# Kernel optimization log

Measured on AMD Instinct MI355X. Metric: run time of the kernel, lower is better.

The kernel has to match this reference:

```python
import jax, jax.numpy as jnp
import numpy as np

NP, NC, E, EL = 50000, 5000, 200000, 100000
DP, DC, HID, OUT, HEADS = 1280, 256, 128, 128, 4


def setup_inputs() -> dict:
    key = jax.random.key(0)
    ks = jax.random.split(key, 40)
    p = lambda k, shp: jax.random.normal(k, shp, dtype=jnp.float32) * 0.05
    inp = {
        "x_protein": jax.random.normal(ks[0], (NP, DP), dtype=jnp.float32),
        "x_class": jax.random.normal(ks[1], (NC, DC), dtype=jnp.float32),
        "src": jax.random.randint(ks[2], (E,), 0, NP),
        "dst": jax.random.randint(ks[3], (E,), 0, NC),
        "edge_label_src": jax.random.randint(ks[4], (EL,), 0, NP),
        "edge_label_dst": jax.random.randint(ks[5], (EL,), 0, NC),
        # SAGEConv, relation protein->class (updates class nodes)
        "sage_pc_Wl": p(ks[6], (DP, HID)), "sage_pc_bl": p(ks[7], (HID,)), "sage_pc_Wr": p(ks[8], (DC, HID)),
        # SAGEConv, relation class->protein (updates protein nodes)
        "sage_cp_Wl": p(ks[9], (DC, HID)), "sage_cp_bl": p(ks[10], (HID,)), "sage_cp_Wr": p(ks[11], (DP, HID)),
        # GATConv p->c (inputs are hidden after conv1)
        "gat_pc_Wsrc": p(ks[12], (HID, HEADS * HID)), "gat_pc_Wdst": p(ks[13], (HID, HEADS * HID)),
        "gat_pc_asrc": p(ks[14], (HEADS, HID)), "gat_pc_adst": p(ks[15], (HEADS, HID)), "gat_pc_b": p(ks[16], (HID,)),
        # GATConv c->p
        "gat_cp_Wsrc": p(ks[17], (HID, HEADS * HID)), "gat_cp_Wdst": p(ks[18], (HID, HEADS * HID)),
        "gat_cp_asrc": p(ks[19], (HEADS, HID)), "gat_cp_adst": p(ks[20], (HEADS, HID)), "gat_cp_b": p(ks[21], (HID,)),
        # final per-node-type Linear (to_hetero duplicates lin per node type)
        "lin_p_W": p(ks[22], (HID, OUT)), "lin_p_b": p(ks[23], (OUT,)),
        "lin_c_W": p(ks[24], (HID, OUT)), "lin_c_b": p(ks[25], (OUT,)),
        # link predictor
        "link_W": p(ks[26], (2 * OUT, 1)), "link_b": p(ks[27], (1,)),
    }
    return inp


def _sage(x_src, x_dst, s, d, Wl, bl, Wr, n_dst):
    # PyG SAGEConv: lin_l(mean_aggr(x_src)) + lin_r(x_dst); lin_l has bias.
    agg = jax.ops.segment_sum(x_src[s], d, num_segments=n_dst)
    cnt = jax.ops.segment_sum(jnp.ones((s.shape[0], 1), x_src.dtype), d, num_segments=n_dst)
    mean = agg / jnp.maximum(cnt, 1.0)
    return mean @ Wl + bl + x_dst @ Wr


def _gat(x_src, x_dst, s, d, Ws, Wd, a_s, a_d, b, n_dst):
    # PyG GATConv bipartite, heads=HEADS, concat=False, add_self_loops=False.
    H, C = a_s.shape
    hs = (x_src @ Ws).reshape(-1, H, C)   # [Ns, H, C]
    hd = (x_dst @ Wd).reshape(-1, H, C)   # [Nd, H, C]
    als = jnp.einsum('nhc,hc->nh', hs, a_s)
    ald = jnp.einsum('nhc,hc->nh', hd, a_d)
    e = jax.nn.leaky_relu(als[s] + ald[d], 0.2)                    # [E, H]
    emax = jax.ops.segment_max(e, d, num_segments=n_dst)          # stable softmax per dst
    ee = jnp.exp(e - emax[d])
    denom = jax.ops.segment_sum(ee, d, num_segments=n_dst)
    alpha = ee / denom[d]                                          # [E, H]
    out = jax.ops.segment_sum(alpha[:, :, None] * hs[s], d, num_segments=n_dst)  # [Nd, H, C]
    return out.mean(axis=1) + b  # concat=False -> mean over heads


def reference(x_protein, x_class, src, dst, edge_label_src, edge_label_dst,
              sage_pc_Wl, sage_pc_bl, sage_pc_Wr,
              sage_cp_Wl, sage_cp_bl, sage_cp_Wr,
              gat_pc_Wsrc, gat_pc_Wdst, gat_pc_asrc, gat_pc_adst, gat_pc_b,
              gat_cp_Wsrc, gat_cp_Wdst, gat_cp_asrc, gat_cp_adst, gat_cp_b,
              lin_p_W, lin_p_b, lin_c_W, lin_c_b, link_W, link_b):
    # Layer 1: hetero SAGE (each node type has exactly one incoming relation)
    h_c = jax.nn.relu(_sage(x_protein, x_class, src, dst, sage_pc_Wl, sage_pc_bl, sage_pc_Wr, NC))
    h_p = jax.nn.relu(_sage(x_class, x_protein, dst, src, sage_cp_Wl, sage_cp_bl, sage_cp_Wr, NP))
    # Layer 2: hetero GAT
    g_c = jax.nn.relu(_gat(h_p, h_c, src, dst, gat_pc_Wsrc, gat_pc_Wdst, gat_pc_asrc, gat_pc_adst, gat_pc_b, NC))
    g_p = jax.nn.relu(_gat(h_c, h_p, dst, src, gat_cp_Wsrc, gat_cp_Wdst, gat_cp_asrc, gat_cp_adst, gat_cp_b, NP))
    # Per-type output projection
    z_p = g_p @ lin_p_W + lin_p_b
    z_c = g_c @ lin_c_W + lin_c_b
    # Link predictor: gather, concat, linear, sigmoid
    ef = jnp.concatenate([z_p[edge_label_src], z_c[edge_label_dst]], axis=-1)  # [EL, 2*OUT]
    return jax.nn.sigmoid(ef @ link_W + link_b).squeeze(-1)
```

## Files before the change

### kernel.cpp

```cpp
#include <hip/hip_runtime.h>
#include <math.h>

#define NPROT 50000
#define NCLS  5000
#define DIMP  1280
#define DIMC  256
#define SCAN_N (NCLS + NPROT)

#define P1B  ((NPROT+63)/64)
#define C1BY ((NCLS+63)/64)
#define C1B  (4*C1BY)

typedef float4 f4;
typedef __attribute__((ext_vector_type(8))) short short8;
typedef __attribute__((ext_vector_type(4))) float f32x4;

__device__ __forceinline__ unsigned short f2bf(float f){
    unsigned u = __float_as_uint(f);
    u += 0x7FFFu + ((u >> 16) & 1u);
    return (unsigned short)(u >> 16);
}
__device__ __forceinline__ float bf2f(unsigned short b){
    return __uint_as_float(((unsigned)b) << 16);
}
__device__ __forceinline__ void gload_lds16(const void* g, void* l){
    __builtin_amdgcn_global_load_lds((const __attribute__((address_space(1))) void*)g,
                                     (__attribute__((address_space(3))) void*)l, 16, 0, 0);
}
__device__ __forceinline__ int OFFV(const int* __restrict__ offv, const int* __restrict__ part, int v){
    return offv[v] + part[v>>10];
}

__global__ __launch_bounds__(256) void mega1(const float* __restrict__ Af,
                                             const unsigned short* __restrict__ BtP,
                                             unsigned short* __restrict__ P1,
                                             const float* __restrict__ Ac,
                                             const float* __restrict__ WcatC,
                                             float* __restrict__ C1,
                                             const int* __restrict__ src, const int* __restrict__ dst,
                                             const int* __restrict__ offv, const int* __restrict__ part,
                                             int* __restrict__ cur, int* __restrict__ adj, int E){
    __shared__ __align__(16) unsigned char smem[24*1024];
    const int blk = blockIdx.x;
    const int tid = threadIdx.x;

    if(blk < P1B){
        unsigned char* As = smem;
        unsigned char* Bs = smem + 8*1024;
        const int lane = tid & 63;
        const int w    = tid >> 6;
        const int row0 = blk * 64;
        const int kg = lane >> 4, fr = lane & 15;

        f32x4 acc[4][4] = {};

        for(int k0 = 0; k0 < DIMP; k0 += 32){
            #pragma unroll
            for(int i=0;i<2;i++){
                int c  = i*256 + tid;
                int r  = c >> 3, cc = c & 7;
                int scc = cc ^ (r & 7);
                int srow = min(row0 + r, NPROT-1);
                gload_lds16((const void*)(Af + (size_t)srow*DIMP + k0 + scc*4),
                            (void*)(As + (i*256 + (tid & ~63))*16));
            }
            #pragma unroll
            for(int i=0;i<4;i++){
                int c  = i*256 + tid;
                int r  = c >> 2, cc = c & 3;
                int scc = cc ^ ((r>>1) & 3);
                gload_lds16((const void*)(BtP + (size_t)r*DIMP + k0 + scc*8),
                            (void*)(Bs + (i*256 + (tid & ~63))*16));
            }
            __syncthreads();

            short8 aF[4], bF[4];
            #pragma unroll
            for(int m=0;m<4;m++){
                int r = m*16 + fr;
                int b0 = r*128 + kg*32;
                f4 lo = *(const f4*)(As + (( b0      ) ^ ((r&7)<<4)));
                f4 hi = *(const f4*)(As + (( b0 + 16 ) ^ ((r&7)<<4)));
                union { short8 s; unsigned short u[8]; } uu;
                uu.u[0]=f2bf(lo.x); uu.u[1]=f2bf(lo.y); uu.u[2]=f2bf(lo.z); uu.u[3]=f2bf(lo.w);
                uu.u[4]=f2bf(hi.x); uu.u[5]=f2bf(hi.y); uu.u[6]=f2bf(hi.z); uu.u[7]=f2bf(hi.w);
                aF[m] = uu.s;
            }
            #pragma unroll
            for(int n=0;n<4;n++){
                int r = w*64 + n*16 + fr;
                int b0 = (r*64 + kg*16) ^ (((r>>1)&3)<<4);
                bF[n] = *(const short8*)(Bs + b0);
            }
            #pragma unroll
            for(int m=0;m<4;m++)
            #pragma unroll
            for(int n=0;n<4;n++)
                acc[m][n] = __builtin_amdgcn_mfma_f32_16x16x32_bf16(aF[m], bF[n], acc[m][n], 0, 0, 0);
            __syncthreads();
        }

        #pragma unroll
        for(int m=0;m<4;m++)
        #pragma unroll
        for(int r=0;r<4;r++){
            int row = row0 + m*16 + kg*4 + r;
            if(row < NPROT){
                #pragma unroll
                for(int n=0;n<4;n++)
                    P1[(size_t)row*256 + w*64 + n*16 + fr] = f2bf(acc[m][n][r]);
            }
        }
    } else if(blk < P1B + C1B){
        float (*As)[68] = (float(*)[68])smem;
        float (*Bs)[64] = (float(*)[64])(smem + 16*68*4);
        const int bi = blk - P1B;
        const int row0 = (bi >> 2) * 64;
        const int col0 = (bi & 3) * 64;
        const int ty = tid >> 4;
        const int tx = tid & 15;
        const int m  = tid >> 2;
        const int kq = (tid & 3) << 2;
        const int kb = tid >> 4;
        const int c4 = (tid & 15) << 2;

        float acc[4][4];
        #pragma unroll
        for(int i=0;i<4;i++)
        #pragma unroll
            for(int j=0;j<4;j++) acc[i][j]=0.f;

        const bool arow_ok = (row0 + m) < NCLS;
        const float* Abase = Ac + (size_t)(row0 + m) * DIMC + kq;
        const float* Bbase = WcatC + col0 + c4 + (size_t)kb * 256;

        for(int k0 = 0; k0 < DIMC; k0 += 16){
            f4 av;
            if(arow_ok) av = *(const f4*)(Abase + k0);
            else        av = make_float4(0.f,0.f,0.f,0.f);
            As[kq+0][m]=av.x; As[kq+1][m]=av.y; As[kq+2][m]=av.z; As[kq+3][m]=av.w;
            *(f4*)&Bs[kb][c4] = *(const f4*)(Bbase + (size_t)k0 * 256);
            __syncthreads();
            #pragma unroll
            for(int kk=0;kk<16;kk++){
                f4 a = *(const f4*)&As[kk][ty<<2];
                f4 b = *(const f4*)&Bs[kk][tx<<2];
                float ar[4]={a.x,a.y,a.z,a.w};
                float br[4]={b.x,b.y,b.z,b.w};
                #pragma unroll
                for(int i=0;i<4;i++)
                #pragma unroll
                    for(int j=0;j<4;j++) acc[i][j] += ar[i]*br[j];
            }
            __syncthreads();
        }
        #pragma unroll
        for(int i=0;i<4;i++){
            int r = row0 + (ty<<2) + i;
            if(r < NCLS){
                f4 v = make_float4(acc[i][0],acc[i][1],acc[i][2],acc[i][3]);
                *(f4*)&C1[(size_t)r*256 + col0 + (tx<<2)] = v;
            }
        }
    } else {
        int e = (blk - P1B - C1B)*256 + tid;
        if(e < E){
            int s = src[e], d = dst[e];
            int pc = atomicAdd(&cur[d],1);        adj[OFFV(offv,part,d)+pc] = s;
            int pp = atomicAdd(&cur[NCLS+s],1);   adj[OFFV(offv,part,NCLS+s)+pp] = d;
        }
    }
}

#define NPB ((NPROT+127)/128)
#define NCB ((NCLS+127)/128)
__global__ __launch_bounds__(256) void gemm_hs(const unsigned short* __restrict__ Ap,
                                               const unsigned short* __restrict__ Ac,
                                               const unsigned short* __restrict__ Btp,
                                               const unsigned short* __restrict__ Btc,
                                               const float* __restrict__ projP,
                                               const float* __restrict__ projC,
                                               unsigned short* __restrict__ Cp,
                                               unsigned short* __restrict__ Cc,
                                               float* __restrict__ attP,
                                               float* __restrict__ attC){
    const bool cls = (int)blockIdx.y >= NPB;
    const unsigned short* A  = cls ? Ac : Ap;
    const unsigned short* Bt = cls ? Btc : Btp;
    unsigned short* C = cls ? Cc : Cp;
    const int M = cls ? NCLS : NPROT;
    const int row0 = (cls ? blockIdx.y - NPB : blockIdx.y) * 128;
    const int col0 = blockIdx.x * 128;

    __shared__ __align__(16) unsigned char As[128*32*2];
    __shared__ __align__(16) unsigned char Bs[128*32*2];
    __shared__ float projS[1024];
    const int tid  = threadIdx.x;
    const int lane = tid & 63;
    const int w    = tid >> 6;
    const int wm   = w >> 1, wn = w & 1;
    const int kg = lane >> 4, fr = lane & 15;

    f32x4 acc[4][4] = {};

    for(int k0 = 0; k0 < 128; k0 += 32){
        #pragma unroll
        for(int i=0;i<2;i++){
            int c  = i*256 + w*64 + lane;
            int r  = c >> 2, cc = c & 3;
            int scc = cc ^ ((r>>1) & 3);
            int srow = min(row0 + r, M-1);
            gload_lds16((const void*)(A + (size_t)srow*128 + k0 + scc*8),
                        (void*)(As + (i*256 + w*64)*16));
        }
        #pragma unroll
        for(int i=0;i<2;i++){
            int c  = i*256 + w*64 + lane;
            int r  = c >> 2, cc = c & 3;
            int scc = cc ^ ((r>>1) & 3);
            gload_lds16((const void*)(Bt + (size_t)(col0 + r)*128 + k0 + scc*8),
                        (void*)(Bs + (i*256 + w*64)*16));
        }
        __syncthreads();

        short8 aF[4], bF[4];
        #pragma unroll
        for(int m=0;m<4;m++){
            int r = wm*64 + m*16 + fr;
            int b0 = (r*64 + kg*16) ^ (((r>>1)&3)<<4);
            aF[m] = *(const short8*)(As + b0);
        }
        #pragma unroll
        for(int n=0;n<4;n++){
            int r = wn*64 + n*16 + fr;
            int b0 = (r*64 + kg*16) ^ (((r>>1)&3)<<4);
            bF[n] = *(const short8*)(Bs + b0);
        }
        #pragma unroll
        for(int m=0;m<4;m++)
        #pragma unroll
        for(int n=0;n<4;n++)
            acc[m][n] = __builtin_amdgcn_mfma_f32_16x16x32_bf16(aF[m], bF[n], acc[m][n], 0, 0, 0);
        __syncthreads();
    }

    #pragma unroll
    for(int m=0;m<4;m++)
    #pragma unroll
    for(int r=0;r<4;r++){
        int row = row0 + wm*64 + m*16 + kg*4 + r;
        if(row < M){
            #pragma unroll
            for(int n=0;n<4;n++)
                C[(size_t)row*512 + col0 + wn*64 + n*16 + fr] = f2bf(acc[m][n][r]);
        }
    }

    if(blockIdx.x == 0){
        const float* proj = cls ? projC : projP;
        float* att = cls ? attC : attP;
        for(int i=tid;i<1024;i+=256) projS[i] = proj[i];
        __syncthreads();
        int ri = tid >> 1, cb = (tid & 1)*4;
        int row = row0 + ri;
        if(row < M){
            const unsigned short* ar = A + (size_t)row*128;
            float s0=0.f,s1=0.f,s2=0.f,s3=0.f;
            #pragma unroll
            for(int kk=0;kk<16;kk++){
                short8 a8 = *(const short8*)(ar + kk*8);
                #pragma unroll
                for(int q=0;q<8;q++){
                    float av = bf2f((unsigned short)a8[q]);
                    const float* pr = &projS[(kk*8+q)*8 + cb];
                    s0 += av*pr[0]; s1 += av*pr[1]; s2 += av*pr[2]; s3 += av*pr[3];
                }
            }
            f4 o = make_float4(s0,s1,s2,s3);
            *(f4*)&att[(size_t)row*8 + cb] = o;
        }
    }
}

__global__ void setup(const float* __restrict__ Wl_pc, const float* __restrict__ Wr_cp,
                      const float* __restrict__ Wl_cp, const float* __restrict__ Wr_pc,
                      const float* __restrict__ pcWs, const float* __restrict__ pcAs,
                      const float* __restrict__ pcWd, const float* __restrict__ pcAd,
                      const float* __restrict__ cpWs, const float* __restrict__ cpAs,
                      const float* __restrict__ cpWd, const float* __restrict__ cpAd,
                      const float* __restrict__ lpW, const float* __restrict__ lpb,
                      const float* __restrict__ lcW, const float* __restrict__ lcb,
                      const float* __restrict__ linkW,
                      const int* __restrict__ src, const int* __restrict__ dst,
                      unsigned short* __restrict__ BtP, float* __restrict__ WcatC,
                      unsigned short* __restrict__ BtSp, unsigned short* __restrict__ BtSc,
                      float* __restrict__ projP, float* __restrict__ projC,
                      float* __restrict__ w_p, float* __restrict__ w_c,
                      float* __restrict__ cpc,
                      int* __restrict__ deg, int E){
    int blk = blockIdx.x, tid = threadIdx.x;
    if(blk < 2048){
        int t = blk*256 + tid;
        if(t < 327680){
            int n = t / 1280, k = t % 1280;
            float v = (n<128) ? Wl_pc[(size_t)k*128+n] : Wr_cp[(size_t)k*128+n-128];
            BtP[t] = f2bf(v);
        } else if(t < 393216){
            int i = t - 327680; int k = i>>8, j = i&255;
            WcatC[i] = (j<128) ? Wl_cp[(size_t)k*128+j] : Wr_pc[(size_t)k*128+j-128];
        } else if(t < 458752){
            int i = t - 393216; int n = i>>7, k = i&127;
            BtSp[i] = f2bf(pcWs[(size_t)k*512+n]);
        } else {
            int i = t - 458752; int n = i>>7, k = i&127;
            BtSc[i] = f2bf(cpWs[(size_t)k*512+n]);
        }
    } else if(blk < 2056){
        int sec = (blk-2048) >> 1;
        int t = ((blk-2048) & 1)*256 + tid;
        const float *W, *a; float* proj; int colbase;
        if(sec==0){ W=pcWs; a=pcAs; proj=projP; colbase=0; }
        else if(sec==1){ W=cpWd; a=cpAd; proj=projP; colbase=4; }
        else if(sec==2){ W=pcWd; a=pcAd; proj=projC; colbase=0; }
        else { W=cpWs; a=cpAs; proj=projC; colbase=4; }
        int k = t >> 2, h = t & 3;
        const float* w = W + (size_t)k*512 + h*128;
        const float* av = a + h*128;
        float s=0.f;
        for(int c=0;c<128;c++) s += w[c]*av[c];
        proj[k*8 + colbase + h] = s;
    } else if(blk == 2056){
        if(tid < 128){
            float s=0.f;
            for(int o=0;o<128;o++) s += lpW[(size_t)tid*128+o]*linkW[o];
            w_p[tid]=s;
        } else {
            int j=tid-128;
            float s=0.f;
            for(int o=0;o<128;o++) s += lcW[(size_t)j*128+o]*linkW[128+o];
            w_c[j]=s;
        }
        if(tid==0){ float s=0.f; for(int o=0;o<128;o++) s+=lpb[o]*linkW[o];      cpc[0]=s; }
        if(tid==1){ float s=0.f; for(int o=0;o<128;o++) s+=lcb[o]*linkW[128+o];  cpc[1]=s; }
    } else {
        int e = (blk-2057)*256 + tid;
        if(e < E){
            atomicAdd(&deg[dst[e]],1);
            atomicAdd(&deg[NCLS + src[e]],1);
        }
    }
}

__global__ __launch_bounds__(1024) void scan1(const int* __restrict__ in, int* __restrict__ out,
                                              int* __restrict__ part, int n){
    __shared__ int buf[1024];
    int tid = threadIdx.x;
    int g = blockIdx.x*1024 + tid;
    int v = (g<n) ? in[g] : 0;
    buf[tid] = v;
    __syncthreads();
    for(int o=1;o<1024;o<<=1){
        int t = (tid>=o) ? buf[tid-o] : 0;
        __syncthreads();
        buf[tid] += t;
        __syncthreads();
    }
    if(g<n) out[g] = buf[tid] - v;
    if(tid==1023) part[blockIdx.x] = buf[1023];
}
__global__ __launch_bounds__(64) void scan2(int* __restrict__ part, int nb,
                                            int* __restrict__ offv, int n){
    int tid = threadIdx.x;
    int orig = (tid<nb) ? part[tid] : 0;
    int v = orig;
    #pragma unroll
    for(int o=1;o<64;o<<=1){
        int t = __shfl_up(v, o);
        if(tid>=o) v += t;
    }
    int total = __shfl(v, nb-1);
    if(tid<nb) part[tid] = v - orig;
    if(tid == (n>>10)) offv[n] = total - (v - orig);
}

__global__ __launch_bounds__(256) void sage_all(const int* __restrict__ offv, const int* __restrict__ part,
                                                const int* __restrict__ adj,
                                                const unsigned short* __restrict__ P1, const float* __restrict__ C1,
                                                const float* __restrict__ bl_pc, const float* __restrict__ bl_cp,
                                                unsigned short* __restrict__ h_c, unsigned short* __restrict__ h_p){
    int v = blockIdx.x*4 + (threadIdx.x>>6);
    int l = threadIdx.x & 63;
    if(v >= SCAN_N) return;
    int b = OFFV(offv,part,v), deg = OFFV(offv,part,v+1)-b;
    float a0=0.f, a1=0.f;
    float inv = 1.f/(float)max(deg,1);
    if(v < NCLS){
        for(int i=0;i<deg;i++){
            int s = adj[b+i];
            ushort2 w = *((const ushort2*)P1 + (size_t)s*128 + l);
            a0 += bf2f(w.x); a1 += bf2f(w.y);
        }
        float2 sv = *((const float2*)C1 + (size_t)v*128 + 64 + l);
        float h0 = fmaxf(a0*inv + bl_pc[2*l]   + sv.x, 0.f);
        float h1 = fmaxf(a1*inv + bl_pc[2*l+1] + sv.y, 0.f);
        ushort2 o; o.x=f2bf(h0); o.y=f2bf(h1);
        *((ushort2*)h_c + (size_t)v*64 + l) = o;
    } else {
        int m = v - NCLS;
        for(int i=0;i<deg;i++){
            int d = adj[b+i];
            float2 w = *((const float2*)C1 + (size_t)d*128 + l);
            a0 += w.x; a1 += w.y;
        }
        ushort2 sv = *((const ushort2*)P1 + (size_t)m*128 + 64 + l);
        float h0 = fmaxf(a0*inv + bl_cp[2*l]   + bf2f(sv.x), 0.f);
        float h1 = fmaxf(a1*inv + bl_cp[2*l+1] + bf2f(sv.y), 0.f);
        ushort2 o; o.x=f2bf(h0); o.y=f2bf(h1);
        *((ushort2*)h_p + (size_t)m*64 + l) = o;
    }
}

__global__ __launch_bounds__(128) void gat_all(const int* __restrict__ offv, const int* __restrict__ part,
                                               const int* __restrict__ adj,
                                               const float* __restrict__ attP, const float* __restrict__ attC,
                                               const unsigned short* __restrict__ hs_p,
                                               const unsigned short* __restrict__ hs_c,
                                               const float* __restrict__ gb_pc, const float* __restrict__ gb_cp,
                                               const float* __restrict__ w_c, const float* __restrict__ w_p,
                                               const float* __restrict__ cpc,
                                               float* __restrict__ u_c, float* __restrict__ u_p){
    __shared__ float ald[4];
    __shared__ int   adjS[32];
    __shared__ float eeS[32*4];
    __shared__ float den8[8];
    __shared__ f4    red4[32];

    int n = blockIdx.x;
    const bool cls = n < NCLS;
    const int node = cls ? n : n - NCLS;
    const float* attS = cls ? attP : attC;
    const float* attD = cls ? attC : attP;
    const int abase = cls ? 0 : 4;
    const unsigned short* hs = cls ? hs_p : hs_c;
    const float* gb = cls ? gb_pc : gb_cp;
    const float* wv = cls ? w_c : w_p;
    float* u = cls ? u_c : u_p;
    const int cidx = cls ? 1 : 0;

    int j = threadIdx.x;
    const int hh = j >> 5;
    const int q  = j & 31;
    int b = OFFV(offv,part,n), deg = OFFV(offv,part,n+1)-b;
    if(j < 4) ald[j] = attD[(size_t)node*8 + abase + j];

    float a0=0.f, a1=0.f, a2=0.f, a3=0.f;
    float denP = 0.f;

    for(int base=0; base<deg; base+=32){
        int cnt = min(32, deg-base);
        if(j < cnt) adjS[j] = adj[b+base+j];
        __syncthreads();
        if(j < cnt*4){
            int i = j>>2, h = j&3;
            int s = adjS[i];
            float e = attS[(size_t)s*8 + abase + h] + ald[h];
            e = e > 0.f ? e : 0.2f*e;
            float ee = __expf(e);
            eeS[j] = ee;
            denP += ee;
        }
        __syncthreads();
        for(int ii=0; ii<cnt; ii++){
            int s = adjS[ii];
            float ee = eeS[ii*4 + hh];
            ushort4 v = *(const ushort4*)(hs + (size_t)s*512 + hh*128 + q*4);
            a0 += ee*bf2f(v.x); a1 += ee*bf2f(v.y);
            a2 += ee*bf2f(v.z); a3 += ee*bf2f(v.w);
        }
        __syncthreads();
    }

    float dp = denP;
    dp += __shfl_xor(dp, 4);
    dp += __shfl_xor(dp, 8);
    dp += __shfl_xor(dp, 16);
    dp += __shfl_xor(dp, 32);
    if((j & 63) < 4) den8[(j>>6)*4 + (j&3)] = dp;
    __syncthreads();

    float den_h = den8[hh] + den8[4+hh];
    float inv = (deg > 0) ? 0.25f/den_h : 0.f;
    a0 *= inv; a1 *= inv; a2 *= inv; a3 *= inv;

    a0 += __shfl_xor(a0, 32); a1 += __shfl_xor(a1, 32);
    a2 += __shfl_xor(a2, 32); a3 += __shfl_xor(a3, 32);
    if(j >= 64 && j < 96) red4[q] = make_float4(a0,a1,a2,a3);
    __syncthreads();
    float val = 0.f;
    if(j < 32){
        f4 r = red4[q];
        float t0 = a0 + r.x, t1 = a1 + r.y, t2 = a2 + r.z, t3 = a3 + r.w;
        const float* gbq = gb + q*4;
        const float* wvq = wv + q*4;
        val = fmaxf(t0 + gbq[0], 0.f)*wvq[0]
            + fmaxf(t1 + gbq[1], 0.f)*wvq[1]
            + fmaxf(t2 + gbq[2], 0.f)*wvq[2]
            + fmaxf(t3 + gbq[3], 0.f)*wvq[3];
    }
    #pragma unroll
    for(int o=16;o;o>>=1) val += __shfl_down(val, o);
    if(j == 0) u[node] = val + cpc[cidx];
}

__global__ void link_out(const int* __restrict__ els, const int* __restrict__ eld,
                         const float* __restrict__ u_p, const float* __restrict__ u_c,
                         const float* __restrict__ linkb, float* __restrict__ out, int EL){
    int i = blockIdx.x*256 + threadIdx.x;
    if(i >= EL) return;
    float x = u_p[els[i]] + u_c[eld[i]] + linkb[0];
    out[i] = 1.f/(1.f + __expf(-x));
}

extern "C" void kernel_launch(void* const* d_in, const int* in_sizes, int n_in,
                              void* d_out, int out_size, void* d_ws, size_t ws_size,
                              hipStream_t stream){
    const float* x_p  = (const float*)d_in[0];
    const float* x_c  = (const float*)d_in[1];
    const int*   src  = (const int*)d_in[2];
    const int*   dst  = (const int*)d_in[3];
    const int*   els  = (const int*)d_in[4];
    const int*   eld  = (const int*)d_in[5];
    const float* sage_pc_Wl = (const float*)d_in[6];
    const float* sage_pc_bl = (const float*)d_in[7];
    const float* sage_pc_Wr = (const float*)d_in[8];
    const float* sage_cp_Wl = (const float*)d_in[9];
    const float* sage_cp_bl = (const float*)d_in[10];
    const float* sage_cp_Wr = (const float*)d_in[11];
    const float* gat_pc_Wsrc = (const float*)d_in[12];
    const float* gat_pc_Wdst = (const float*)d_in[13];
    const float* gat_pc_asrc = (const float*)d_in[14];
    const float* gat_pc_adst = (const float*)d_in[15];
    const float* gat_pc_b    = (const float*)d_in[16];
    const float* gat_cp_Wsrc = (const float*)d_in[17];
    const float* gat_cp_Wdst = (const float*)d_in[18];
    const float* gat_cp_asrc = (const float*)d_in[19];
    const float* gat_cp_adst = (const float*)d_in[20];
    const float* gat_cp_b    = (const float*)d_in[21];
    const float* lin_p_W = (const float*)d_in[22];
    const float* lin_p_b = (const float*)d_in[23];
    const float* lin_c_W = (const float*)d_in[24];
    const float* lin_c_b = (const float*)d_in[25];
    const float* link_W  = (const float*)d_in[26];
    const float* link_b  = (const float*)d_in[27];

    const int E  = in_sizes[2];
    const int EL = in_sizes[4];

    float* ws = (float*)d_ws;
    size_t off = 0;
    auto alloc = [&](size_t n)->float*{ float* p = ws + off; off += (n + 3) & ~(size_t)3; return p; };

    unsigned short* BtP  = (unsigned short*)alloc((size_t)256*DIMP/2);
    float* WcatC = alloc((size_t)DIMC*256);
    unsigned short* BtSp = (unsigned short*)alloc((size_t)512*128/2);
    unsigned short* BtSc = (unsigned short*)alloc((size_t)512*128/2);
    unsigned short* P1   = (unsigned short*)alloc((size_t)NPROT*256/2);
    float* C1    = alloc((size_t)NCLS*256);
    unsigned short* h_p  = (unsigned short*)alloc((size_t)NPROT*128/2);
    unsigned short* h_c  = (unsigned short*)alloc((size_t)NCLS*128/2);
    unsigned short* hs_p = (unsigned short*)alloc((size_t)NPROT*512/2);
    unsigned short* hs_c = (unsigned short*)alloc((size_t)NCLS*512/2);
    float* attP  = alloc((size_t)NPROT*8);
    float* attC  = alloc((size_t)NCLS*8);
    float* projP = alloc(128*8);
    float* projC = alloc(128*8);
    float* w_p   = alloc(128);
    float* w_c   = alloc(128);
    float* cpc   = alloc(4);
    int* degcur = (int*)alloc((size_t)2*SCAN_N);
    int* deg = degcur;
    int* cur = degcur + SCAN_N;
    int* offv = (int*)alloc(SCAN_N+1);
    int* part = (int*)alloc(64);
    int* adj  = (int*)alloc((size_t)2*E);
    float* u_p = alloc(NPROT);
    float* u_c = alloc(NCLS);
    if(off*4 > ws_size) return;

    hipMemsetAsync(degcur, 0, (size_t)2*SCAN_N*4, stream);

    setup<<<2057 + (E+255)/256, 256, 0, stream>>>(
        sage_pc_Wl, sage_cp_Wr, sage_cp_Wl, sage_pc_Wr,
        gat_pc_Wsrc, gat_pc_asrc, gat_pc_Wdst, gat_pc_adst,
        gat_cp_Wsrc, gat_cp_asrc, gat_cp_Wdst, gat_cp_adst,
        lin_p_W, lin_p_b, lin_c_W, lin_c_b, link_W,
        src, dst,
        BtP, WcatC, BtSp, BtSc, projP, projC, w_p, w_c, cpc, deg, E);

    const int NB = (SCAN_N + 1023)/1024;
    scan1<<<NB,1024,0,stream>>>(deg, offv, part, SCAN_N);
    scan2<<<1,64,0,stream>>>(part, NB, offv, SCAN_N);

    const int FILLB = (E+255)/256;
    mega1<<<P1B + C1B + FILLB, 256, 0, stream>>>(x_p, BtP, P1, x_c, WcatC, C1,
                                                 src, dst, offv, part, cur, adj, E);

    sage_all<<<(SCAN_N+3)/4,256,0,stream>>>(offv, part, adj, P1, C1, sage_pc_bl, sage_cp_bl, h_c, h_p);

    gemm_hs<<<dim3(4,NPB+NCB),256,0,stream>>>(h_p, h_c, BtSp, BtSc, projP, projC,
                                              hs_p, hs_c, attP, attC);

    gat_all<<<SCAN_N,128,0,stream>>>(offv, part, adj, attP, attC, hs_p, hs_c,
                                     gat_pc_b, gat_cp_b, w_c, w_p, cpc, u_c, u_p);

    link_out<<<(EL+255)/256,256,0,stream>>>(els, eld, u_p, u_c, link_b, (float*)d_out, EL);
}
```

Measured before the change: 337.6 us.

## Double-buffer protein GEMM in mega1 with 128-row tiles and 512 threads

The protein projection GEMM inside mega1 now uses 128-row tiles across 8 waves (a 2x4 wave grid), so each B tile loaded into LDS is reused across twice as many rows. Its K loop is double-buffered: the next stage's global-to-LDS loads are issued while MFMAs run on the current buffer, which hides load latency. To fit the 512-thread launch, the class GEMM branch idles its upper half of threads and the edge-fill branch covers 512 edges per block. LDS grows to 64KB per block, which can lower occupancy, and half the threads in the class blocks do no work.

Measured after the change: 318.0 us. 1.06x faster.

```diff
diff --git a/kernel.cpp b/kernel.cpp
--- a/kernel.cpp
+++ b/kernel.cpp
@@ -6,8 +6,9 @@
 #define DIMP  1280
 #define DIMC  256
 #define SCAN_N (NCLS + NPROT)
-
-#define P1B  ((NPROT+63)/64)
+#define KSTEPS (DIMP/32)
+
+#define P1B  ((NPROT+127)/128)
 #define C1BY ((NCLS+63)/64)
 #define C1B  (4*C1BY)
 
@@ -31,7 +32,7 @@
     return offv[v] + part[v>>10];
 }
 
-__global__ __launch_bounds__(256) void mega1(const float* __restrict__ Af,
+__global__ __launch_bounds__(512) void mega1(const float* __restrict__ Af,
                                              const unsigned short* __restrict__ BtP,
                                              unsigned short* __restrict__ P1,
                                              const float* __restrict__ Ac,
@@ -40,47 +41,59 @@
                                              const int* __restrict__ src, const int* __restrict__ dst,
                                              const int* __restrict__ offv, const int* __restrict__ part,
                                              int* __restrict__ cur, int* __restrict__ adj, int E){
-    __shared__ __align__(16) unsigned char smem[24*1024];
+    __shared__ __align__(16) unsigned char smem[64*1024];
     const int blk = blockIdx.x;
     const int tid = threadIdx.x;
 
     if(blk < P1B){
         unsigned char* As = smem;
-        unsigned char* Bs = smem + 8*1024;
+        unsigned char* Bs = smem + 32*1024;
         const int lane = tid & 63;
         const int w    = tid >> 6;
-        const int row0 = blk * 64;
+        const int wm   = w >> 2, wn = w & 3;
+        const int row0 = blk * 128;
         const int kg = lane >> 4, fr = lane & 15;
 
         f32x4 acc[4][4] = {};
 
-        for(int k0 = 0; k0 < DIMP; k0 += 32){
+        auto STAGE = [&](int buf, int k0){
+            unsigned char* Ab = As + buf*16384;
+            unsigned char* Bb = Bs + buf*16384;
             #pragma unroll
             for(int i=0;i<2;i++){
-                int c  = i*256 + tid;
+                int c  = i*512 + tid;
                 int r  = c >> 3, cc = c & 7;
                 int scc = cc ^ (r & 7);
                 int srow = min(row0 + r, NPROT-1);
                 gload_lds16((const void*)(Af + (size_t)srow*DIMP + k0 + scc*4),
-                            (void*)(As + (i*256 + (tid & ~63))*16));
-            }
-            #pragma unroll
-            for(int i=0;i<4;i++){
-                int c  = i*256 + tid;
+                            (void*)(Ab + (i*512 + w*64 + lane)*16));
+            }
+            #pragma unroll
+            for(int i=0;i<2;i++){
+                int c  = i*512 + tid;
                 int r  = c >> 2, cc = c & 3;
                 int scc = cc ^ ((r>>1) & 3);
                 gload_lds16((const void*)(BtP + (size_t)r*DIMP + k0 + scc*8),
-                            (void*)(Bs + (i*256 + (tid & ~63))*16));
-            }
-            __syncthreads();
+                            (void*)(Bb + (i*512 + w*64 + lane)*16));
+            }
+        };
+
+        STAGE(0, 0);
+        __syncthreads();
+
+        for(int t=0; t<KSTEPS; ++t){
+            const int cb = t & 1;
+            if(t+1 < KSTEPS) STAGE(cb^1, (t+1)*32);
+            const unsigned char* Ab = As + cb*16384;
+            const unsigned char* Bb = Bs + cb*16384;
 
             short8 aF[4], bF[4];
             #pragma unroll
             for(int m=0;m<4;m++){
-                int r = m*16 + fr;
+                int r = wm*64 + m*16 + fr;
                 int b0 = r*128 + kg*32;
-                f4 lo = *(const f4*)(As + (( b0      ) ^ ((r&7)<<4)));
-                f4 hi = *(const f4*)(As + (( b0 + 16 ) ^ ((r&7)<<4)));
+                f4 lo = *(const f4*)(Ab + (( b0      ) ^ ((r&7)<<4)));
+                f4 hi = *(const f4*)(Ab + (( b0 + 16 ) ^ ((r&7)<<4)));
                 union { short8 s; unsigned short u[8]; } uu;
                 uu.u[0]=f2bf(lo.x); uu.u[1]=f2bf(lo.y); uu.u[2]=f2bf(lo.z); uu.u[3]=f2bf(lo.w);
                 uu.u[4]=f2bf(hi.x); uu.u[5]=f2bf(hi.y); uu.u[6]=f2bf(hi.z); uu.u[7]=f2bf(hi.w);
@@ -88,9 +101,9 @@
             }
             #pragma unroll
             for(int n=0;n<4;n++){
-                int r = w*64 + n*16 + fr;
+                int r = wn*64 + n*16 + fr;
                 int b0 = (r*64 + kg*16) ^ (((r>>1)&3)<<4);
-                bF[n] = *(const short8*)(Bs + b0);
+                bF[n] = *(const short8*)(Bb + b0);
             }
             #pragma unroll
             for(int m=0;m<4;m++)
@@ -104,11 +117,11 @@
         for(int m=0;m<4;m++)
         #pragma unroll
         for(int r=0;r<4;r++){
-            int row = row0 + m*16 + kg*4 + r;
+            int row = row0 + wm*64 + m*16 + kg*4 + r;
             if(row < NPROT){
                 #pragma unroll
                 for(int n=0;n<4;n++)
-                    P1[(size_t)row*256 + w*64 + n*16 + fr] = f2bf(acc[m][n][r]);
+                    P1[(size_t)row*256 + wn*64 + n*16 + fr] = f2bf(acc[m][n][r]);
             }
         }
     } else if(blk < P1B + C1B){
@@ -117,6 +130,7 @@
         const int bi = blk - P1B;
         const int row0 = (bi >> 2) * 64;
         const int col0 = (bi & 3) * 64;
+        const bool act = tid < 256;
         const int ty = tid >> 4;
         const int tx = tid & 15;
         const int m  = tid >> 2;
@@ -130,40 +144,46 @@
         #pragma unroll
             for(int j=0;j<4;j++) acc[i][j]=0.f;
 
-        const bool arow_ok = (row0 + m) < NCLS;
-        const float* Abase = Ac + (size_t)(row0 + m) * DIMC + kq;
+        const bool arow_ok = act && (row0 + m) < NCLS;
+        const float* Abase = Ac + (size_t)(row0 + min(m,255)) * DIMC + kq;
         const float* Bbase = WcatC + col0 + c4 + (size_t)kb * 256;
 
         for(int k0 = 0; k0 < DIMC; k0 += 16){
-            f4 av;
-            if(arow_ok) av = *(const f4*)(Abase + k0);
-            else        av = make_float4(0.f,0.f,0.f,0.f);
-            As[kq+0][m]=av.x; As[kq+1][m]=av.y; As[kq+2][m]=av.z; As[kq+3][m]=av.w;
-            *(f4*)&Bs[kb][c4] = *(const f4*)(Bbase + (size_t)k0 * 256);
+            if(act){
+                f4 av;
+                if(arow_ok) av = *(const f4*)(Abase + k0);
+                else        av = make_float4(0.f,0.f,0.f,0.f);
+                As[kq+0][m]=av.x; As[kq+1][m]=av.y; As[kq+2][m]=av.z; As[kq+3][m]=av.w;
+                *(f4*)&Bs[kb][c4] = *(const f4*)(Bbase + (size_t)k0 * 256);
+            }
             __syncthreads();
-            #pragma unroll
-            for(int kk=0;kk<16;kk++){
-                f4 a = *(const f4*)&As[kk][ty<<2];
-                f4 b = *(const f4*)&Bs[kk][tx<<2];
-                float ar[4]={a.x,a.y,a.z,a.w};
-                float br[4]={b.x,b.y,b.z,b.w};
+            if(act){
                 #pragma unroll
-                for(int i=0;i<4;i++)
-                #pragma unroll
-                    for(int j=0;j<4;j++) acc[i][j] += ar[i]*br[j];
+                for(int kk=0;kk<16;kk++){
+                    f4 a = *(const f4*)&As[kk][ty<<2];
+                    f4 b = *(const f4*)&Bs[kk][tx<<2];
+                    float ar[4]={a.x,a.y,a.z,a.w};
+                    float br[4]={b.x,b.y,b.z,b.w};
+                    #pragma unroll
+                    for(int i=0;i<4;i++)
+                    #pragma unroll
+                        for(int j=0;j<4;j++) acc[i][j] += ar[i]*br[j];
+                }
             }
             __syncthreads();
         }
-        #pragma unroll
-        for(int i=0;i<4;i++){
-            int r = row0 + (ty<<2) + i;
-            if(r < NCLS){
-                f4 v = make_float4(acc[i][0],acc[i][1],acc[i][2],acc[i][3]);
-                *(f4*)&C1[(size_t)r*256 + col0 + (tx<<2)] = v;
+        if(act){
+            #pragma unroll
+            for(int i=0;i<4;i++){
+                int r = row0 + (ty<<2) + i;
+                if(r < NCLS){
+                    f4 v = make_float4(acc[i][0],acc[i][1],acc[i][2],acc[i][3]);
+                    *(f4*)&C1[(size_t)r*256 + col0 + (tx<<2)] = v;
+                }
             }
         }
     } else {
-        int e = (blk - P1B - C1B)*256 + tid;
+        int e = (blk - P1B - C1B)*512 + tid;
         if(e < E){
             int s = src[e], d = dst[e];
             int pc = atomicAdd(&cur[d],1);        adj[OFFV(offv,part,d)+pc] = s;
@@ -601,8 +621,8 @@
     scan1<<<NB,1024,0,stream>>>(deg, offv, part, SCAN_N);
     scan2<<<1,64,0,stream>>>(part, NB, offv, SCAN_N);
 
-    const int FILLB = (E+255)/256;
-    mega1<<<P1B + C1B + FILLB, 256, 0, stream>>>(x_p, BtP, P1, x_c, WcatC, C1,
+    const int FILLB = (E+511)/512;
+    mega1<<<P1B + C1B + FILLB, 512, 0, stream>>>(x_p, BtP, P1, x_c, WcatC, C1,
                                                  src, dst, offv, part, cur, adj, E);
 
     sage_all<<<(SCAN_N+3)/4,256,0,stream>>>(offv, part, adj, P1, C1, sage_pc_bl, sage_cp_bl, h_c, h_p);
```

## Load MFMA fragments straight from global memory and store C1 as bf16

Applied to the files above, without the earlier changes.

The protein GEMM in mega1 no longer stages A and B tiles through LDS with global_load_lds and block barriers. Each lane now reads its fragments directly from global memory, with unroll 2 and a launch-bounds occupancy hint of 4. C1 is also stored as bf16 instead of fp32, which halves its size and the traffic of the gathers in sage_all. The risks are poorer coalescing and more redundant global reads with no LDS reuse, plus some loss of precision in C1.

After: 453.0 us. +34.2%, slower.

```diff
diff --git a/kernel.cpp b/kernel.cpp
--- a/kernel.cpp
+++ b/kernel.cpp
@@ -31,22 +31,21 @@
     return offv[v] + part[v>>10];
 }
 
-__global__ __launch_bounds__(256) void mega1(const float* __restrict__ Af,
-                                             const unsigned short* __restrict__ BtP,
-                                             unsigned short* __restrict__ P1,
-                                             const float* __restrict__ Ac,
-                                             const float* __restrict__ WcatC,
-                                             float* __restrict__ C1,
-                                             const int* __restrict__ src, const int* __restrict__ dst,
-                                             const int* __restrict__ offv, const int* __restrict__ part,
-                                             int* __restrict__ cur, int* __restrict__ adj, int E){
-    __shared__ __align__(16) unsigned char smem[24*1024];
+__global__ __launch_bounds__(256,4) void mega1(const float* __restrict__ Af,
+                                               const unsigned short* __restrict__ BtP,
+                                               unsigned short* __restrict__ P1,
+                                               const float* __restrict__ Ac,
+                                               const float* __restrict__ WcatC,
+                                               unsigned short* __restrict__ C1,
+                                               const int* __restrict__ src, const int* __restrict__ dst,
+                                               const int* __restrict__ offv, const int* __restrict__ part,
+                                               int* __restrict__ cur, int* __restrict__ adj, int E){
+    __shared__ __align__(16) float As64[16][68];
+    __shared__ __align__(16) float Bs64[16][64];
     const int blk = blockIdx.x;
     const int tid = threadIdx.x;
 
     if(blk < P1B){
-        unsigned char* As = smem;
-        unsigned char* Bs = smem + 8*1024;
         const int lane = tid & 63;
         const int w    = tid >> 6;
         const int row0 = blk * 64;
@@ -54,50 +53,36 @@
 
         f32x4 acc[4][4] = {};
 
-        for(int k0 = 0; k0 < DIMP; k0 += 32){
-            #pragma unroll
-            for(int i=0;i<2;i++){
-                int c  = i*256 + tid;
-                int r  = c >> 3, cc = c & 7;
-                int scc = cc ^ (r & 7);
-                int srow = min(row0 + r, NPROT-1);
-                gload_lds16((const void*)(Af + (size_t)srow*DIMP + k0 + scc*4),
-                            (void*)(As + (i*256 + (tid & ~63))*16));
-            }
-            #pragma unroll
-            for(int i=0;i<4;i++){
-                int c  = i*256 + tid;
-                int r  = c >> 2, cc = c & 3;
-                int scc = cc ^ ((r>>1) & 3);
-                gload_lds16((const void*)(BtP + (size_t)r*DIMP + k0 + scc*8),
-                            (void*)(Bs + (i*256 + (tid & ~63))*16));
-            }
-            __syncthreads();
-
+        const float* aB[4];
+        const unsigned short* bB[4];
+        #pragma unroll
+        for(int m=0;m<4;m++){
+            int r = min(row0 + m*16 + fr, NPROT-1);
+            aB[m] = Af + (size_t)r*DIMP + kg*8;
+        }
+        #pragma unroll
+        for(int n=0;n<4;n++)
+            bB[n] = BtP + (size_t)(w*64 + n*16 + fr)*DIMP + kg*8;
+
+        #pragma unroll 2
+        for(int ko=0; ko<DIMP; ko+=32){
             short8 aF[4], bF[4];
             #pragma unroll
+            for(int n=0;n<4;n++) bF[n] = *(const short8*)(bB[n] + ko);
+            #pragma unroll
             for(int m=0;m<4;m++){
-                int r = m*16 + fr;
-                int b0 = r*128 + kg*32;
-                f4 lo = *(const f4*)(As + (( b0      ) ^ ((r&7)<<4)));
-                f4 hi = *(const f4*)(As + (( b0 + 16 ) ^ ((r&7)<<4)));
+                f4 lo = *(const f4*)(aB[m] + ko);
+                f4 hi = *(const f4*)(aB[m] + ko + 4);
                 union { short8 s; unsigned short u[8]; } uu;
                 uu.u[0]=f2bf(lo.x); uu.u[1]=f2bf(lo.y); uu.u[2]=f2bf(lo.z); uu.u[3]=f2bf(lo.w);
                 uu.u[4]=f2bf(hi.x); uu.u[5]=f2bf(hi.y); uu.u[6]=f2bf(hi.z); uu.u[7]=f2bf(hi.w);
                 aF[m] = uu.s;
             }
             #pragma unroll
-            for(int n=0;n<4;n++){
-                int r = w*64 + n*16 + fr;
-                int b0 = (r*64 + kg*16) ^ (((r>>1)&3)<<4);
-                bF[n] = *(const short8*)(Bs + b0);
-            }
-            #pragma unroll
             for(int m=0;m<4;m++)
             #pragma unroll
             for(int n=0;n<4;n++)
                 acc[m][n] = __builtin_amdgcn_mfma_f32_16x16x32_bf16(aF[m], bF[n], acc[m][n], 0, 0, 0);
-            __syncthreads();
         }
 
         #pragma unroll
@@ -112,8 +97,6 @@
             }
         }
     } else if(blk < P1B + C1B){
-        float (*As)[68] = (float(*)[68])smem;
-        float (*Bs)[64] = (float(*)[64])(smem + 16*68*4);
         const int bi = blk - P1B;
         const int row0 = (bi >> 2) * 64;
         const int col0 = (bi & 3) * 64;
@@ -138,13 +121,13 @@
             f4 av;
             if(arow_ok) av = *(const f4*)(Abase + k0);
             else        av = make_float4(0.f,0.f,0.f,0.f);
-            As[kq+0][m]=av.x; As[kq+1][m]=av.y; As[kq+2][m]=av.z; As[kq+3][m]=av.w;
-            *(f4*)&Bs[kb][c4] = *(const f4*)(Bbase + (size_t)k0 * 256);
+            As64[kq+0][m]=av.x; As64[kq+1][m]=av.y; As64[kq+2][m]=av.z; As64[kq+3][m]=av.w;
+            *(f4*)&Bs64[kb][c4] = *(const f4*)(Bbase + (size_t)k0 * 256);
             __syncthreads();
             #pragma unroll
             for(int kk=0;kk<16;kk++){
-                f4 a = *(const f4*)&As[kk][ty<<2];
-                f4 b = *(const f4*)&Bs[kk][tx<<2];
+                f4 a = *(const f4*)&As64[kk][ty<<2];
+                f4 b = *(const f4*)&Bs64[kk][tx<<2];
                 float ar[4]={a.x,a.y,a.z,a.w};
                 float br[4]={b.x,b.y,b.z,b.w};
                 #pragma unroll
@@ -158,8 +141,10 @@
         for(int i=0;i<4;i++){
             int r = row0 + (ty<<2) + i;
             if(r < NCLS){
-                f4 v = make_float4(acc[i][0],acc[i][1],acc[i][2],acc[i][3]);
-                *(f4*)&C1[(size_t)r*256 + col0 + (tx<<2)] = v;
+                ushort4 v;
+                v.x=f2bf(acc[i][0]); v.y=f2bf(acc[i][1]);
+                v.z=f2bf(acc[i][2]); v.w=f2bf(acc[i][3]);
+                *(ushort4*)&C1[(size_t)r*256 + col0 + (tx<<2)] = v;
             }
         }
     } else {
@@ -385,7 +370,8 @@
 
 __global__ __launch_bounds__(256) void sage_all(const int* __restrict__ offv, const int* __restrict__ part,
                                                 const int* __restrict__ adj,
-                                                const unsigned short* __restrict__ P1, const float* __restrict__ C1,
+                                                const unsigned short* __restrict__ P1,
+                                                const unsigned short* __restrict__ C1,
                                                 const float* __restrict__ bl_pc, const float* __restrict__ bl_cp,
                                                 unsigned short* __restrict__ h_c, unsigned short* __restrict__ h_p){
     int v = blockIdx.x*4 + (threadIdx.x>>6);
@@ -400,17 +386,17 @@
             ushort2 w = *((const ushort2*)P1 + (size_t)s*128 + l);
             a0 += bf2f(w.x); a1 += bf2f(w.y);
         }
-        float2 sv = *((const float2*)C1 + (size_t)v*128 + 64 + l);
-        float h0 = fmaxf(a0*inv + bl_pc[2*l]   + sv.x, 0.f);
-        float h1 = fmaxf(a1*inv + bl_pc[2*l+1] + sv.y, 0.f);
+        ushort2 sv = *((const ushort2*)C1 + (size_t)v*128 + 64 + l);
+        float h0 = fmaxf(a0*inv + bl_pc[2*l]   + bf2f(sv.x), 0.f);
+        float h1 = fmaxf(a1*inv + bl_pc[2*l+1] + bf2f(sv.y), 0.f);
         ushort2 o; o.x=f2bf(h0); o.y=f2bf(h1);
         *((ushort2*)h_c + (size_t)v*64 + l) = o;
     } else {
         int m = v - NCLS;
         for(int i=0;i<deg;i++){
             int d = adj[b+i];
-            float2 w = *((const float2*)C1 + (size_t)d*128 + l);
-            a0 += w.x; a1 += w.y;
+            ushort2 w = *((const ushort2*)C1 + (size_t)d*128 + l);
+            a0 += bf2f(w.x); a1 += bf2f(w.y);
         }
         ushort2 sv = *((const ushort2*)P1 + (size_t)m*128 + 64 + l);
         float h0 = fmaxf(a0*inv + bl_cp[2*l]   + bf2f(sv.x), 0.f);
@@ -565,7 +551,7 @@
     unsigned short* BtSp = (unsigned short*)alloc((size_t)512*128/2);
     unsigned short* BtSc = (unsigned short*)alloc((size_t)512*128/2);
     unsigned short* P1   = (unsigned short*)alloc((size_t)NPROT*256/2);
-    float* C1    = alloc((size_t)NCLS*256);
+    unsigned short* C1   = (unsigned short*)alloc((size_t)NCLS*256/2);
     unsigned short* h_p  = (unsigned short*)alloc((size_t)NPROT*128/2);
     unsigned short* h_c  = (unsigned short*)alloc((size_t)NCLS*128/2);
     unsigned short* hs_p = (unsigned short*)alloc((size_t)NPROT*512/2);
```
